# Performance work log

Hardware: AMD Instinct MI355X
Metric: run time of the kernel (lower is better)

The kernel has to match this reference:

```python
import jax, jax.numpy as jnp
import numpy as np

WIDTH = 64
HEIGHT = 64
FEAT = 128
LAT = 64
NUM_SLOTS = 7


def pixel_coords(img_size):
    g = jnp.linspace(-1.0, 1.0, img_size)
    g1, g2 = jnp.meshgrid(g, g, indexing='ij')  # matches torch.meshgrid default
    return jnp.stack([g1, g2], axis=0)[None]  # (1, 2, S, S)


def clamp_pg(x, lo, hi):
    # clamp that preserves gradients (straight-through)
    return x + jax.lax.stop_gradient(jnp.clip(x, lo, hi) - x)


def setup_inputs() -> dict:
    key = jax.random.key(0)
    k0, k1, k2, k3 = jax.random.split(key, 4)
    bs = 64
    x = jax.random.normal(k0, (bs, FEAT, WIDTH, HEIGHT), jnp.float32)
    rand_pixel = jax.random.uniform(k1, (bs, 1, WIDTH, HEIGHT), jnp.float32)
    conv_w = jax.random.normal(k2, (LAT, FEAT), jnp.float32) / np.sqrt(FEAT)
    conv_b = jax.random.normal(k3, (LAT,), jnp.float32) * 0.01
    gate = jnp.asarray(0.5, jnp.float32)  # ScalarGate parameter (nonzero so c_f is non-degenerate)
    # laplacian kernel: sigma_init = 1 / (sqrt(num_slots) * log 2)
    log_sigma = jnp.asarray(np.log(1.0 / (np.sqrt(NUM_SLOTS) * np.log(2.0))), jnp.float32)
    return {'x': x, 'rand_pixel': rand_pixel, 'conv_w': conv_w, 'conv_b': conv_b,
            'gate': gate, 'log_sigma': log_sigma, 'num_cl_steps': 6}


def _forward(x, rand_pixel, conv_w, conv_b, gate, log_sigma, num_cl_steps):
    bs = x.shape[0]
    # SemiConv: gated 1x1 conv + fixed uv coordinate channels
    out = gate * (jnp.einsum('of,bfhw->bohw', conv_w, x) + conv_b[None, :, None, None])
    uv = jnp.concatenate([jnp.zeros((1, LAT - 2, WIDTH, HEIGHT), out.dtype),
                          pixel_coords(WIDTH).astype(out.dtype)], axis=1)
    c_f = out + uv                      # (bs, LAT, W, H)
    delta = out[:, -2:]                 # (bs, 2, W, H)
    sigma = jnp.exp(log_sigma)
    c_flat = c_f.reshape(bs, LAT, -1)   # (bs, LAT, W*H)
    b_idx = jnp.arange(bs)
    log_s0 = jnp.zeros((bs, 1, WIDTH, HEIGHT), c_f.dtype)

    def step(log_s, _):
        # interpolate-to-same-size is identity -> scope = exp(log_s)
        probs = (rand_pixel * jnp.exp(log_s)).reshape(bs, -1)
        idx = jnp.argmax(probs, axis=1)                 # (bs,)
        seed = c_flat[b_idx, :, idx]                    # (bs, LAT)
        diff = c_f - seed[:, :, None, None]
        dist = jnp.sqrt(clamp_pg((diff ** 2).sum(1), 1e-10, 1e10))  # euclidian (laplacian kernel)
        alpha = jnp.exp(-dist / sigma)[:, None]         # (bs, 1, W, H)
        alpha = clamp_pg(alpha, 0.01, 0.99)
        log_m = log_s + jnp.log(alpha)
        new_log_s = log_s + jnp.log1p(-alpha)
        return new_log_s, (log_m, new_log_s, seed)

    log_s_final, (log_m_steps, log_s_steps, seeds) = jax.lax.scan(
        step, log_s0, None, length=num_cl_steps)
    # log_m_k has num_cl_steps masks plus the final scope appended
    log_m_k = jnp.concatenate([log_m_steps, log_s_final[None]], axis=0)
    log_s_k = jnp.concatenate([log_s0[None], log_s_steps], axis=0)
    return log_m_k, log_s_k, c_f, delta, seeds


def reference(x, rand_pixel, conv_w, conv_b, gate, log_sigma, num_cl_steps):
    return _forward(x, rand_pixel, conv_w, conv_b, gate, log_sigma, num_cl_steps)
```

## Files before the change

kernel.cpp:

```cpp
#include <hip/hip_runtime.h>
#include <hip/hip_bf16.h>

#define NPIX 4096
#define FEAT 128
#define LAT 64
#define BS 64
#define NSTEPS 6

#define OFF_LOGM  0u
#define OFF_LOGS  1835008u
#define OFF_CF    3670016u
#define OFF_DELTA 20447232u
#define OFF_SEEDS 20971520u

typedef float f32x4 __attribute__((ext_vector_type(4)));
typedef short s16x8 __attribute__((ext_vector_type(8)));

__device__ __forceinline__ void amax_comb(float& bv, int& bi, float v, int i) {
    if (v > bv || (v == bv && i < bi)) { bv = v; bi = i; }
}

__device__ __forceinline__ short f2bf_rne(float r) {
    __hip_bfloat16 h = __float2bfloat16(r);
    return __builtin_bit_cast(short, h);
}

__device__ __forceinline__ void split2(float v, short& hi, short& lo) {
    unsigned u = __builtin_bit_cast(unsigned, v);
    hi = (short)(u >> 16);
    float hf = __builtin_bit_cast(float, u & 0xFFFF0000u);
    lo = f2bf_rne(v - hf);
}

__device__ __forceinline__ void transpose4(float4& v, int b) {
    float4 w;
    w.x = __shfl_xor(v.x, 1, 64); w.y = __shfl_xor(v.y, 1, 64);
    w.z = __shfl_xor(v.z, 1, 64); w.w = __shfl_xor(v.w, 1, 64);
    float4 u;
    if ((b & 1) == 0) u = make_float4(v.x, w.x, v.z, w.z);
    else              u = make_float4(w.y, v.y, w.w, v.w);
    float4 w2;
    w2.x = __shfl_xor(u.x, 2, 64); w2.y = __shfl_xor(u.y, 2, 64);
    w2.z = __shfl_xor(u.z, 2, 64); w2.w = __shfl_xor(u.w, 2, 64);
    if ((b & 2) == 0) v = make_float4(u.x, u.y, w2.x, w2.y);
    else              v = make_float4(w2.z, w2.w, u.z, u.w);
}

__global__ void prep_w(const float* __restrict__ w, const float* __restrict__ gate_p,
                       short* __restrict__ gwh, short* __restrict__ gwl)
{
    int i = blockIdx.x * 256 + threadIdx.x;
    float v = gate_p[0] * w[i];
    short h, l; split2(v, h, l);
    gwh[i] = h; gwl[i] = l;
}

__global__ __launch_bounds__(512, 4) void conv_mfma(
    const float* __restrict__ x, const float* __restrict__ rand_pixel,
    const float* __restrict__ bias, const float* __restrict__ gate_p,
    float* __restrict__ out,
    float* __restrict__ pval, int* __restrict__ pidx, int* __restrict__ cnt,
    const short* __restrict__ gwh, const short* __restrict__ gwl)
{
    __shared__ __align__(16) short Whi[64][132];
    __shared__ __align__(16) short Wlo[64][132];
    __shared__ float sbias[64];

    const int tid  = threadIdx.x;
    const int b    = blockIdx.x >> 4;
    const int tile = blockIdx.x & 15;
    const int p0   = tile * 256;
    const int lane = tid & 63;
    const int wv   = tid >> 6;
    const int l15  = lane & 15;
    const int lg   = lane >> 4;
    const int oh   = wv >> 2;
    const int pxq  = wv & 3;
    const int j    = lane & 3;

    if (tile == 0 && tid < 8) cnt[b * 8 + tid] = 0;
    if (tid < 64) sbias[tid] = gate_p[0] * bias[tid];

    {
        const int o = tid >> 3, c = (tid & 7) * 16;
        *(s16x8*)&Whi[o][c]     = *(const s16x8*)&gwh[o * 128 + c];
        *(s16x8*)&Whi[o][c + 8] = *(const s16x8*)&gwh[o * 128 + c + 8];
        *(s16x8*)&Wlo[o][c]     = *(const s16x8*)&gwl[o * 128 + c];
        *(s16x8*)&Wlo[o][c + 8] = *(const s16x8*)&gwl[o * 128 + c + 8];
    }
    __syncthreads();

    f32x4 acc[2][4];
    #pragma unroll
    for (int og2 = 0; og2 < 2; ++og2)
        #pragma unroll
        for (int pg = 0; pg < 4; ++pg)
            acc[og2][pg] = (f32x4){0.f, 0.f, 0.f, 0.f};

    const float* xb = x + (size_t)b * FEAT * NPIX + p0 + pxq * 64 + (l15 & ~3);

    #pragma unroll
    for (int kc = 0; kc < 4; ++kc) {
        float4 t[4][2];
        #pragma unroll
        for (int pg = 0; pg < 4; ++pg) {
            const float* xp = xb + (size_t)(kc * 32 + lg * 8 + j) * NPIX + pg * 16;
            t[pg][0] = *(const float4*)(xp);
            t[pg][1] = *(const float4*)(xp + (size_t)4 * NPIX);
        }

        s16x8 Ah[2], Al[2];
        #pragma unroll
        for (int og2 = 0; og2 < 2; ++og2) {
            int o = oh * 32 + og2 * 16 + l15;
            Ah[og2] = *(const s16x8*)&Whi[o][kc * 32 + lg * 8];
            Al[og2] = *(const s16x8*)&Wlo[o][kc * 32 + lg * 8];
        }

        #pragma unroll
        for (int pg = 0; pg < 4; ++pg) {
            float4 t0 = t[pg][0];
            float4 t1 = t[pg][1];
            transpose4(t0, j);
            transpose4(t1, j);
            s16x8 Bh, Bl;
            short h, l;
            split2(t0.x, h, l); Bh[0] = h; Bl[0] = l;
            split2(t0.y, h, l); Bh[1] = h; Bl[1] = l;
            split2(t0.z, h, l); Bh[2] = h; Bl[2] = l;
            split2(t0.w, h, l); Bh[3] = h; Bl[3] = l;
            split2(t1.x, h, l); Bh[4] = h; Bl[4] = l;
            split2(t1.y, h, l); Bh[5] = h; Bl[5] = l;
            split2(t1.z, h, l); Bh[6] = h; Bl[6] = l;
            split2(t1.w, h, l); Bh[7] = h; Bl[7] = l;
            #pragma unroll
            for (int og2 = 0; og2 < 2; ++og2) {
                acc[og2][pg] = __builtin_amdgcn_mfma_f32_16x16x32_bf16(Ah[og2], Bh, acc[og2][pg], 0, 0, 0);
                acc[og2][pg] = __builtin_amdgcn_mfma_f32_16x16x32_bf16(Ah[og2], Bl, acc[og2][pg], 0, 0, 0);
                acc[og2][pg] = __builtin_amdgcn_mfma_f32_16x16x32_bf16(Al[og2], Bh, acc[og2][pg], 0, 0, 0);
            }
        }
    }

    float* cf = out + OFF_CF + (size_t)b * LAT * NPIX;
    #pragma unroll
    for (int og2 = 0; og2 < 2; ++og2) {
        #pragma unroll
        for (int pg = 0; pg < 4; ++pg) {
            #pragma unroll
            for (int r = 0; r < 4; ++r) {
                int o = oh * 32 + og2 * 16 + lg * 4 + r;
                int p = p0 + pxq * 64 + pg * 16 + l15;
                float vv = acc[og2][pg][r] + sbias[o];
                if (o == 62) {
                    out[OFF_DELTA + ((size_t)b * 2 + 0) * NPIX + p] = vv;
                    vv += (float)(-1.0 + 2.0 * (double)(p >> 6) / 63.0);
                } else if (o == 63) {
                    out[OFF_DELTA + ((size_t)b * 2 + 1) * NPIX + p] = vv;
                    vv += (float)(-1.0 + 2.0 * (double)(p & 63) / 63.0);
                }
                cf[(size_t)o * NPIX + p] = vv;
            }
        }
    }

    if (wv == 0) {
        *(float4*)(out + OFF_LOGS + (size_t)b * NPIX + p0 + lane * 4) =
            make_float4(0.f, 0.f, 0.f, 0.f);
        float4 rv = *(const float4*)(rand_pixel + (size_t)b * NPIX + p0 + lane * 4);
        int pb = p0 + lane * 4;
        float bv = rv.x; int bi = pb;
        if (rv.y > bv) { bv = rv.y; bi = pb + 1; }
        if (rv.z > bv) { bv = rv.z; bi = pb + 2; }
        if (rv.w > bv) { bv = rv.w; bi = pb + 3; }
        #pragma unroll
        for (int off = 32; off > 0; off >>= 1) {
            float ov = __shfl_down(bv, off, 64);
            int   oi = __shfl_down(bi, off, 64);
            amax_comb(bv, bi, ov, oi);
        }
        if (lane == 0) { pval[blockIdx.x] = bv; pidx[blockIdx.x] = bi; }
    }
}

#define REP16(OP) OP(0) OP(1) OP(2) OP(3) OP(4) OP(5) OP(6) OP(7) \
                  OP(8) OP(9) OP(10) OP(11) OP(12) OP(13) OP(14) OP(15)

__global__ __launch_bounds__(1024, 4) void steps_fused(
    const float* __restrict__ rand_pixel, const float* __restrict__ log_sigma_p,
    float* __restrict__ out, float* pv, int* pi, int* cnt)
{
    __shared__ float s_mv[16];
    __shared__ int   s_mi[16];
    __shared__ __align__(16) float s_seed[LAT];
    __shared__ float s_rv[16];
    __shared__ int   s_ri[16];

    const int tid  = threadIdx.x;
    const int b    = blockIdx.x >> 2;
    const int tile = blockIdx.x & 3;
    const int p    = tile * 1024 + tid;

    const float* cfb = out + OFF_CF + (size_t)b * LAT * NPIX;

#define DECLR(i) f32x4 r##i;
    REP16(DECLR)
#define LOADR(i) r##i = (f32x4){ cfb[(size_t)(4*i+0)*NPIX + p], cfb[(size_t)(4*i+1)*NPIX + p], \
                                 cfb[(size_t)(4*i+2)*NPIX + p], cfb[(size_t)(4*i+3)*NPIX + p] };
    REP16(LOADR)

    f32x4 aq = r0 * r0;
#define SQR(i) aq += r##i * r##i;
    SQR(1) SQR(2) SQR(3) SQR(4) SQR(5) SQR(6) SQR(7)
    SQR(8) SQR(9) SQR(10) SQR(11) SQR(12) SQR(13) SQR(14) SQR(15)
    const float cr2 = aq[0] + aq[1] + aq[2] + aq[3];

    const float rp    = rand_pixel[(size_t)b * NPIX + p];
    const float sigma = expf(log_sigma_p[0]);
    float ls = 0.f;

    #pragma unroll 1
    for (int s = 0; s < NSTEPS; ++s) {
        if (s > 0) {
            if (tid == 0) {
                while (__hip_atomic_load(&cnt[b * 8 + s], __ATOMIC_ACQUIRE,
                                         __HIP_MEMORY_SCOPE_AGENT) < 4)
                    __builtin_amdgcn_s_sleep(2);
            }
            __syncthreads();
        }
        const int nmerge = (s == 0) ? 16 : 4;
        if (tid < nmerge) {
            s_mv[tid] = __hip_atomic_load(&pv[(s * BS + b) * 16 + tid],
                                          __ATOMIC_RELAXED, __HIP_MEMORY_SCOPE_AGENT);
            s_mi[tid] = __hip_atomic_load(&pi[(s * BS + b) * 16 + tid],
                                          __ATOMIC_RELAXED, __HIP_MEMORY_SCOPE_AGENT);
        }
        __syncthreads();

        float bv = -1.0f; int bi = 0;
        for (int k = 0; k < nmerge; ++k) amax_comb(bv, bi, s_mv[k], s_mi[k]);

        if (tid < LAT) s_seed[tid] = cfb[(size_t)tid * NPIX + bi];
        __syncthreads();
        if (tile == 0 && tid < LAT)
            out[OFF_SEEDS + ((size_t)s * BS + b) * LAT + tid] = s_seed[tid];

        f32x4 dacc = (f32x4){0.f, 0.f, 0.f, 0.f};
        f32x4 sacc = (f32x4){0.f, 0.f, 0.f, 0.f};
#define DOT(i) { f32x4 sv = *(const f32x4*)&s_seed[4*i]; dacc += r##i * sv; sacc += sv * sv; }
        REP16(DOT)
        float dot = dacc[0] + dacc[1] + dacc[2] + dacc[3];
        float s2  = sacc[0] + sacc[1] + sacc[2] + sacc[3];
        float d2  = cr2 + s2 - 2.0f * dot;

        float dist  = sqrtf(fminf(fmaxf(d2, 1e-10f), 1e10f));
        float alpha = expf(-dist / sigma);
        alpha = fminf(fmaxf(alpha, 0.01f), 0.99f);
        float lm  = ls + logf(alpha);
        float lsn = ls + log1pf(-alpha);

        out[OFF_LOGM + ((size_t)s * BS + b) * NPIX + p]       = lm;
        out[OFF_LOGS + ((size_t)(s + 1) * BS + b) * NPIX + p] = lsn;
        ls = lsn;

        if (s == NSTEPS - 1) {
            out[OFF_LOGM + ((size_t)NSTEPS * BS + b) * NPIX + p] = lsn;
        } else {
            float prob = rp * expf(lsn);
            int   idx  = p;
            #pragma unroll
            for (int off = 32; off > 0; off >>= 1) {
                float ov = __shfl_down(prob, off, 64);
                int   oi = __shfl_down(idx, off, 64);
                amax_comb(prob, idx, ov, oi);
            }
            int lane = tid & 63, wid = tid >> 6;
            if (lane == 0) { s_rv[wid] = prob; s_ri[wid] = idx; }
            __syncthreads();
            if (tid == 0) {
                float fb = s_rv[0]; int fi = s_ri[0];
                #pragma unroll
                for (int k = 1; k < 16; ++k) amax_comb(fb, fi, s_rv[k], s_ri[k]);
                __hip_atomic_store(&pv[((s + 1) * BS + b) * 16 + tile], fb,
                                   __ATOMIC_RELAXED, __HIP_MEMORY_SCOPE_AGENT);
                __hip_atomic_store(&pi[((s + 1) * BS + b) * 16 + tile], fi,
                                   __ATOMIC_RELAXED, __HIP_MEMORY_SCOPE_AGENT);
                __hip_atomic_fetch_add(&cnt[b * 8 + s + 1], 1,
                                       __ATOMIC_RELEASE, __HIP_MEMORY_SCOPE_AGENT);
            }
        }
    }
}

__global__ __launch_bounds__(1024, 4) void step_kernel(
    const float* __restrict__ rand_pixel, const float* __restrict__ log_sigma_p,
    float* __restrict__ out, float* pv, int* pi, int step)
{
    __shared__ float s_mv[16];
    __shared__ int   s_mi[16];
    __shared__ __align__(16) float s_seed[LAT];
    __shared__ float s_rv[16];
    __shared__ int   s_ri[16];

    const int tid  = threadIdx.x;
    const int b    = blockIdx.x >> 2;
    const int tile = blockIdx.x & 3;
    const int p    = tile * 1024 + tid;

    const float* cfb = out + OFF_CF + (size_t)b * LAT * NPIX;

    const int nmerge = (step == 0) ? 16 : 4;
    if (tid < nmerge) { s_mv[tid] = pv[(step * BS + b) * 16 + tid];
                        s_mi[tid] = pi[(step * BS + b) * 16 + tid]; }
    __syncthreads();
    float bv = -1.0f; int bi = 0;
    for (int k = 0; k < nmerge; ++k) amax_comb(bv, bi, s_mv[k], s_mi[k]);

    if (tid < LAT) s_seed[tid] = cfb[(size_t)tid * NPIX + bi];
    __syncthreads();
    if (tile == 0 && tid < LAT)
        out[OFF_SEEDS + ((size_t)step * BS + b) * LAT + tid] = s_seed[tid];

    float d2 = 0.f;
    #pragma unroll
    for (int c = 0; c < LAT; ++c) {
        float d = cfb[(size_t)c * NPIX + p] - s_seed[c];
        d2 = fmaf(d, d, d2);
    }
    float dist  = sqrtf(fminf(fmaxf(d2, 1e-10f), 1e10f));
    float sigma = expf(log_sigma_p[0]);
    float alpha = expf(-dist / sigma);
    alpha = fminf(fmaxf(alpha, 0.01f), 0.99f);

    float ls  = out[OFF_LOGS + ((size_t)step * BS + b) * NPIX + p];
    float lm  = ls + logf(alpha);
    float lsn = ls + log1pf(-alpha);

    out[OFF_LOGM + ((size_t)step * BS + b) * NPIX + p]       = lm;
    out[OFF_LOGS + ((size_t)(step + 1) * BS + b) * NPIX + p] = lsn;
    if (step == NSTEPS - 1)
        out[OFF_LOGM + ((size_t)NSTEPS * BS + b) * NPIX + p] = lsn;

    if (step < NSTEPS - 1) {
        float prob = rand_pixel[(size_t)b * NPIX + p] * expf(lsn);
        int   idx  = p;
        #pragma unroll
        for (int off = 32; off > 0; off >>= 1) {
            float ov = __shfl_down(prob, off, 64);
            int   oi = __shfl_down(idx, off, 64);
            amax_comb(prob, idx, ov, oi);
        }
        int lane = tid & 63, wid = tid >> 6;
        if (lane == 0) { s_rv[wid] = prob; s_ri[wid] = idx; }
        __syncthreads();
        if (tid == 0) {
            float fb = s_rv[0]; int fi = s_ri[0];
            #pragma unroll
            for (int k = 1; k < 16; ++k) amax_comb(fb, fi, s_rv[k], s_ri[k]);
            pv[((step + 1) * BS + b) * 16 + tile] = fb;
            pi[((step + 1) * BS + b) * 16 + tile] = fi;
        }
    }
}

extern "C" void kernel_launch(void* const* d_in, const int* in_sizes, int n_in,
                              void* d_out, int out_size, void* d_ws, size_t ws_size,
                              hipStream_t stream) {
    const float* x          = (const float*)d_in[0];
    const float* rand_pixel = (const float*)d_in[1];
    const float* w          = (const float*)d_in[2];
    const float* bias       = (const float*)d_in[3];
    const float* gate       = (const float*)d_in[4];
    const float* log_sigma  = (const float*)d_in[5];

    float* out = (float*)d_out;
    float* pv  = (float*)d_ws;
    int*   pi  = (int*)((char*)d_ws + 24576);
    int*   cnt = (int*)((char*)d_ws + 49152);
    short* gwh = (short*)((char*)d_ws + 51200);
    short* gwl = (short*)((char*)d_ws + 67584);

    prep_w<<<32, 256, 0, stream>>>(w, gate, gwh, gwl);
    conv_mfma<<<1024, 512, 0, stream>>>(x, rand_pixel, bias, gate, out,
                                        pv, pi, cnt, gwh, gwl);

    const float* a0 = rand_pixel; const float* a1 = log_sigma; float* a2 = out;
    float* a3 = pv; int* a4 = pi; int* a5 = cnt;
    void* kp[6] = {(void*)&a0, (void*)&a1, (void*)&a2, (void*)&a3, (void*)&a4, (void*)&a5};
    hipError_t e = hipLaunchCooperativeKernel((const void*)steps_fused,
                                              dim3(256), dim3(1024), kp, 0, stream);
    if (e != hipSuccess) {
        for (int s = 0; s < NSTEPS; ++s)
            step_kernel<<<256, 1024, 0, stream>>>(rand_pixel, log_sigma, out, pv, pi, s);
    }
}
```

Measured before the change: 138.0 us.

## Stage x tiles in LDS via async global_load_lds with double buffering

Replaces the per-wave register loads of x plus the shuffle-based 4x4 transpose with asynchronous global-to-LDS copies into a double-buffered, XOR-swizzled tile. The next channel chunk is prefetched while the current one feeds the MFMAs. The bf16 hi/lo weight fragments now sit in registers loaded straight from global memory instead of an LDS copy. The aim is to overlap memory latency with compute and drop the cross-lane shuffle work. In exchange it adds per-chunk barriers, needs 64KB of LDS, and lowers the launch-bounds occupancy hint from 4 to 2.

```diff
diff --git a/kernel.cpp b/kernel.cpp
--- a/kernel.cpp
+++ b/kernel.cpp
@@ -32,18 +32,10 @@
     lo = f2bf_rne(v - hf);
 }
 
-__device__ __forceinline__ void transpose4(float4& v, int b) {
-    float4 w;
-    w.x = __shfl_xor(v.x, 1, 64); w.y = __shfl_xor(v.y, 1, 64);
-    w.z = __shfl_xor(v.z, 1, 64); w.w = __shfl_xor(v.w, 1, 64);
-    float4 u;
-    if ((b & 1) == 0) u = make_float4(v.x, w.x, v.z, w.z);
-    else              u = make_float4(w.y, v.y, w.w, v.w);
-    float4 w2;
-    w2.x = __shfl_xor(u.x, 2, 64); w2.y = __shfl_xor(u.y, 2, 64);
-    w2.z = __shfl_xor(u.z, 2, 64); w2.w = __shfl_xor(u.w, 2, 64);
-    if ((b & 2) == 0) v = make_float4(u.x, u.y, w2.x, w2.y);
-    else              v = make_float4(w2.z, w2.w, u.z, u.w);
+__device__ __forceinline__ void gld16(const float* g, float* l) {
+    __builtin_amdgcn_global_load_lds(
+        (const __attribute__((address_space(1))) void*)g,
+        (__attribute__((address_space(3))) void*)l, 16, 0, 0);
 }
 
 __global__ void prep_w(const float* __restrict__ w, const float* __restrict__ gate_p,
@@ -55,15 +47,14 @@
     gwh[i] = h; gwl[i] = l;
 }
 
-__global__ __launch_bounds__(512, 4) void conv_mfma(
+__global__ __launch_bounds__(512, 2) void conv_mfma(
     const float* __restrict__ x, const float* __restrict__ rand_pixel,
     const float* __restrict__ bias, const float* __restrict__ gate_p,
     float* __restrict__ out,
     float* __restrict__ pval, int* __restrict__ pidx, int* __restrict__ cnt,
     const short* __restrict__ gwh, const short* __restrict__ gwl)
 {
-    __shared__ __align__(16) short Whi[64][132];
-    __shared__ __align__(16) short Wlo[64][132];
+    __shared__ __align__(16) float Xs[2][32][256];
     __shared__ float sbias[64];
 
     const int tid  = threadIdx.x;
@@ -76,18 +67,29 @@
     const int lg   = lane >> 4;
     const int oh   = wv >> 2;
     const int pxq  = wv & 3;
-    const int j    = lane & 3;
 
     if (tile == 0 && tid < 8) cnt[b * 8 + tid] = 0;
     if (tid < 64) sbias[tid] = gate_p[0] * bias[tid];
 
-    {
-        const int o = tid >> 3, c = (tid & 7) * 16;
-        *(s16x8*)&Whi[o][c]     = *(const s16x8*)&gwh[o * 128 + c];
-        *(s16x8*)&Whi[o][c + 8] = *(const s16x8*)&gwh[o * 128 + c + 8];
-        *(s16x8*)&Wlo[o][c]     = *(const s16x8*)&gwl[o * 128 + c];
-        *(s16x8*)&Wlo[o][c + 8] = *(const s16x8*)&gwl[o * 128 + c + 8];
-    }
+    const float* xb = x + (size_t)b * FEAT * NPIX + p0;
+
+    #pragma unroll
+    for (int i = 0; i < 4; ++i) {
+        int row = wv * 4 + i;
+        gld16(xb + (size_t)row * NPIX + ((lane ^ (row >> 3)) << 2),
+              &Xs[0][row][0]);
+    }
+
+    s16x8 WAh[4][2], WAl[4][2];
+    #pragma unroll
+    for (int kc = 0; kc < 4; ++kc)
+        #pragma unroll
+        for (int og2 = 0; og2 < 2; ++og2) {
+            int o = oh * 32 + og2 * 16 + l15;
+            WAh[kc][og2] = *(const s16x8*)&gwh[o * 128 + kc * 32 + lg * 8];
+            WAl[kc][og2] = *(const s16x8*)&gwl[o * 128 + kc * 32 + lg * 8];
+        }
+
     __syncthreads();
 
     f32x4 acc[2][4];
@@ -97,49 +99,41 @@
         for (int pg = 0; pg < 4; ++pg)
             acc[og2][pg] = (f32x4){0.f, 0.f, 0.f, 0.f};
 
-    const float* xb = x + (size_t)b * FEAT * NPIX + p0 + pxq * 64 + (l15 & ~3);
-
     #pragma unroll
     for (int kc = 0; kc < 4; ++kc) {
-        float4 t[4][2];
+        const int cur = kc & 1;
+        if (kc < 3) {
+            #pragma unroll
+            for (int i = 0; i < 4; ++i) {
+                int row = wv * 4 + i;
+                gld16(xb + (size_t)((kc + 1) * 32 + row) * NPIX
+                          + ((lane ^ (row >> 3)) << 2),
+                      &Xs[cur ^ 1][row][0]);
+            }
+        }
+
         #pragma unroll
         for (int pg = 0; pg < 4; ++pg) {
-            const float* xp = xb + (size_t)(kc * 32 + lg * 8 + j) * NPIX + pg * 16;
-            t[pg][0] = *(const float4*)(xp);
-            t[pg][1] = *(const float4*)(xp + (size_t)4 * NPIX);
-        }
-
-        s16x8 Ah[2], Al[2];
-        #pragma unroll
-        for (int og2 = 0; og2 < 2; ++og2) {
-            int o = oh * 32 + og2 * 16 + l15;
-            Ah[og2] = *(const s16x8*)&Whi[o][kc * 32 + lg * 8];
-            Al[og2] = *(const s16x8*)&Wlo[o][kc * 32 + lg * 8];
-        }
-
-        #pragma unroll
-        for (int pg = 0; pg < 4; ++pg) {
-            float4 t0 = t[pg][0];
-            float4 t1 = t[pg][1];
-            transpose4(t0, j);
-            transpose4(t1, j);
+            const int q  = pxq * 64 + pg * 16 + l15;
+            const int qb = q >> 2, qs = q & 3;
             s16x8 Bh, Bl;
-            short h, l;
-            split2(t0.x, h, l); Bh[0] = h; Bl[0] = l;
-            split2(t0.y, h, l); Bh[1] = h; Bl[1] = l;
-            split2(t0.z, h, l); Bh[2] = h; Bl[2] = l;
-            split2(t0.w, h, l); Bh[3] = h; Bl[3] = l;
-            split2(t1.x, h, l); Bh[4] = h; Bl[4] = l;
-            split2(t1.y, h, l); Bh[5] = h; Bl[5] = l;
-            split2(t1.z, h, l); Bh[6] = h; Bl[6] = l;
-            split2(t1.w, h, l); Bh[7] = h; Bl[7] = l;
+            #pragma unroll
+            for (int e = 0; e < 8; ++e) {
+                int fl = lg * 8 + e;
+                float xv = Xs[cur][fl][(((qb ^ (fl >> 3)) << 2) | qs)];
+                short h, l;
+                split2(xv, h, l);
+                Bh[e] = h; Bl[e] = l;
+            }
             #pragma unroll
             for (int og2 = 0; og2 < 2; ++og2) {
-                acc[og2][pg] = __builtin_amdgcn_mfma_f32_16x16x32_bf16(Ah[og2], Bh, acc[og2][pg], 0, 0, 0);
-                acc[og2][pg] = __builtin_amdgcn_mfma_f32_16x16x32_bf16(Ah[og2], Bl, acc[og2][pg], 0, 0, 0);
-                acc[og2][pg] = __builtin_amdgcn_mfma_f32_16x16x32_bf16(Al[og2], Bh, acc[og2][pg], 0, 0, 0);
-            }
-        }
+                acc[og2][pg] = __builtin_amdgcn_mfma_f32_16x16x32_bf16(WAh[kc][og2], Bh, acc[og2][pg], 0, 0, 0);
+                acc[og2][pg] = __builtin_amdgcn_mfma_f32_16x16x32_bf16(WAh[kc][og2], Bl, acc[og2][pg], 0, 0, 0);
+                acc[og2][pg] = __builtin_amdgcn_mfma_f32_16x16x32_bf16(WAl[kc][og2], Bh, acc[og2][pg], 0, 0, 0);
+            }
+        }
+
+        if (kc < 3) __syncthreads();
     }
 
     float* cf = out + OFF_CF + (size_t)b * LAT * NPIX;
```

Result: faster. 133.7 us (-3.1%).
